# Kernel tuning notes

Hardware: AMD Instinct MI355X
Metric: run time of the kernel (lower is better)

## Reference

```python
import jax, jax.numpy as jnp
import numpy as np

B, N, D, OUT, ED = 8, 256, 128, 128, 1

def setup_inputs() -> dict:
    key = jax.random.key(0)
    ks = jax.random.split(key, 10)
    in2 = 2 * D + ED  # 257
    s = lambda f: 1.0 / np.sqrt(f)
    return {
        "h": jax.random.normal(ks[0], (B, N, D), dtype=jnp.float32),
        "adj": jax.random.randint(ks[1], (B, N, N), 0, 2, dtype=jnp.int32),
        "dist_matrix": jax.random.uniform(ks[2], (B, N, N), dtype=jnp.float32),
        "Wm1": jax.random.uniform(ks[3], (in2, OUT), minval=-s(in2), maxval=s(in2)),
        "bm1": jnp.zeros((OUT,), jnp.float32),
        "Wm2": jax.random.uniform(ks[4], (OUT, OUT), minval=-s(OUT), maxval=s(OUT)),
        "bm2": jnp.zeros((OUT,), jnp.float32),
        "Wa": jax.random.uniform(ks[5], (in2, 1), minval=-s(in2), maxval=s(in2)),
        "ba": jnp.zeros((1,), jnp.float32),
        "Wu": jax.random.uniform(ks[6], (D + OUT, OUT), minval=-s(D + OUT), maxval=s(D + OUT)),
        "bu": jnp.zeros((OUT,), jnp.float32),
    }

def reference(h, adj, dist_matrix, Wm1, bm1, Wm2, bm2, Wa, ba, Wu, bu):
    # h: (B,N,D); adj,dist: (B,N,N)
    Bb, Nn, Dd = h.shape
    h_i = jnp.broadcast_to(h[:, :, None, :], (Bb, Nn, Nn, Dd))
    h_j = jnp.broadcast_to(h[:, None, :, :], (Bb, Nn, Nn, Dd))
    d_ij = dist_matrix[..., None]
    msg_input = jnp.concatenate([h_i, h_j, d_ij], axis=-1)  # (B,N,N,2D+1)
    # message MLP: Linear -> ReLU -> Linear
    msg = jax.nn.relu(msg_input @ Wm1 + bm1) @ Wm2 + bm2    # (B,N,N,OUT)
    # attention MLP: Linear -> LeakyReLU(0.2)
    attn = jax.nn.leaky_relu(msg_input @ Wa + ba, 0.2)      # (B,N,N,1)
    mask = adj[..., None].astype(msg.dtype)                  # (B,N,N,1)
    attn = jnp.where(mask == 0, jnp.asarray(-1e9, attn.dtype), attn)
    attn = jax.nn.softmax(attn, axis=2)                      # softmax over j
    agg = jnp.sum(attn * msg * mask, axis=2)                 # (B,N,OUT)
    h_new = jax.nn.relu(jnp.concatenate([h, agg], axis=-1) @ Wu + bu)
    return h_new
```

## Files before the change

### kernel.cpp

```cpp
#include <hip/hip_runtime.h>

#define NN 256
#define DD 128
#define OC 128

__device__ __forceinline__ float bcastf(float x, int lane) {
    return __int_as_float(__builtin_amdgcn_readlane(__float_as_int(x), lane));
}

__global__ __launch_bounds__(256) void k1_pre(
    const float* __restrict__ h, const float* __restrict__ Wm1,
    const float* __restrict__ Wa, const float* __restrict__ bm1,
    const float* __restrict__ Wu, const float* __restrict__ ba,
    float* __restrict__ pre, float* __restrict__ aiv, float* __restrict__ ajv)
{
    const int tid  = threadIdx.x;
    const int l    = tid & 63;
    const int w    = tid >> 6;
    const int row0 = blockIdx.x * 2;

    const float2* h2 = (const float2*)h;
    float2 hr[2];
    hr[0] = h2[row0 * 64 + l];
    hr[1] = h2[(row0 + 1) * 64 + l];

    if (w == 3) {
        const float2* Wa2 = (const float2*)Wa;
        const float2 wt = Wa2[l], wb = Wa2[64 + l];
        float vi[2], vj[2];
        #pragma unroll
        for (int r = 0; r < 2; ++r) {
            vi[r] = hr[r].x * wt.x + hr[r].y * wt.y;
            vj[r] = hr[r].x * wb.x + hr[r].y * wb.y;
        }
        #pragma unroll
        for (int o = 1; o < 64; o <<= 1) {
            #pragma unroll
            for (int r = 0; r < 2; ++r) {
                vi[r] += __shfl_xor(vi[r], o, 64);
                vj[r] += __shfl_xor(vj[r], o, 64);
            }
        }
        if (l == 0) {
            const float b0 = ba[0];
            #pragma unroll
            for (int r = 0; r < 2; ++r) {
                aiv[row0 + r] = vi[r] + b0;
                ajv[row0 + r] = vj[r];
            }
        }
        return;
    }

    const float2* W2 = (w == 0) ? (const float2*)Wm1
                     : (w == 1) ? (const float2*)Wm1 + DD * 64
                                : (const float2*)Wu;

    float2 acc[2] = {{0.f, 0.f}, {0.f, 0.f}};
    #pragma unroll 8
    for (int m = 0; m < 64; ++m) {
        const float2 w0 = W2[(2 * m) * 64 + l];
        const float2 w1 = W2[(2 * m + 1) * 64 + l];
        #pragma unroll
        for (int r = 0; r < 2; ++r) {
            const float hx = bcastf(hr[r].x, m);
            const float hy = bcastf(hr[r].y, m);
            acc[r].x = fmaf(hx, w0.x, fmaf(hy, w1.x, acc[r].x));
            acc[r].y = fmaf(hx, w0.y, fmaf(hy, w1.y, acc[r].y));
        }
    }
    if (w == 0) {
        const float2 bb = ((const float2*)bm1)[l];
        #pragma unroll
        for (int r = 0; r < 2; ++r) { acc[r].x += bb.x; acc[r].y += bb.y; }
    }
    float2* pre2 = (float2*)pre;
    #pragma unroll
    for (int r = 0; r < 2; ++r)
        pre2[(row0 + r) * 192 + w * 64 + l] = acc[r];
}

__global__ __launch_bounds__(256) void k2_main(
    const int* __restrict__ adj, const float* __restrict__ dist,
    const float* __restrict__ Wm1, const float* __restrict__ Wa,
    const float* __restrict__ pre,
    const float* __restrict__ aiv, const float* __restrict__ ajv,
    const float* __restrict__ Wm2, const float* __restrict__ bm2,
    const float* __restrict__ Wu,  const float* __restrict__ bu,
    float* __restrict__ out)
{
    const int tid  = threadIdx.x;
    const int l    = tid & 63;
    const int wid  = tid >> 6;
    const int r    = wid >> 1;
    const int hf   = wid & 1;
    const int row0 = blockIdx.x * 2;
    const int row  = row0 + r;
    const int b    = row >> 8;

    __shared__ float mx_sh[4], sm_sh[4], sf_sh[2];
    __shared__ float tp_sh[4][128];
    __shared__ float t_sh[2][128];
    __shared__ float agg_sh[2][128];

    const float2 dv2 = ((const float2*)(dist + row * NN))[hf * 64 + l];
    const int2   mk2 = ((const int2*)  (adj  + row * NN))[hf * 64 + l];
    const float2 aj2 = ((const float2*)(ajv  + b   * NN))[hf * 64 + l];
    const float  ai  = aiv[row];
    const float  dc  = Wa[2 * DD];

    float l0 = ai + aj2.x + dv2.x * dc;
    float l1 = ai + aj2.y + dv2.y * dc;
    l0 = (l0 >= 0.f) ? l0 : 0.2f * l0;
    l1 = (l1 >= 0.f) ? l1 : 0.2f * l1;

    float m = fmaxf(mk2.x ? l0 : -1e9f, mk2.y ? l1 : -1e9f);
    #pragma unroll
    for (int o = 1; o < 64; o <<= 1) m = fmaxf(m, __shfl_xor(m, o, 64));
    if (l == 0) mx_sh[wid] = m;
    __syncthreads();
    const float mx = fmaxf(mx_sh[r * 2], mx_sh[r * 2 + 1]);

    const float e0 = mk2.x ? __expf(l0 - mx) : 0.f;
    const float e1 = mk2.y ? __expf(l1 - mx) : 0.f;
    float s = e0 + e1;
    #pragma unroll
    for (int o = 1; o < 64; o <<= 1) s += __shfl_xor(s, o, 64);
    if (l == 0) sm_sh[wid] = s;
    __syncthreads();
    const float esum = sm_sh[r * 2] + sm_sh[r * 2 + 1];
    const float inv  = (esum > 0.f) ? (1.0f / esum) : 0.f;
    const float w0 = e0 * inv, w1 = e1 * inv;

    const float2* pre2 = (const float2*)pre;
    const float2  pa   = pre2[row * 192 + l];
    const float2  wd1  = ((const float2*)Wm1)[2 * DD * 64 + l];
    const float2* pBb  = pre2 + (size_t)b * NN * 192 + 64 + (size_t)hf * 128 * 192;

    float2 acc = make_float2(0.f, 0.f);
    #pragma unroll 8
    for (int p = 0; p < 64; ++p) {
        const float w0p = bcastf(w0, p);
        const float w1p = bcastf(w1, p);
        const float d0p = bcastf(dv2.x, p);
        const float d1p = bcastf(dv2.y, p);
        const float2 pb0 = pBb[(2 * p) * 192 + l];
        const float2 pb1 = pBb[(2 * p + 1) * 192 + l];
        float vx = fmaf(d0p, wd1.x, pa.x + pb0.x);
        float vy = fmaf(d0p, wd1.y, pa.y + pb0.y);
        acc.x = fmaf(w0p, fmaxf(vx, 0.f), acc.x);
        acc.y = fmaf(w0p, fmaxf(vy, 0.f), acc.y);
        vx = fmaf(d1p, wd1.x, pa.x + pb1.x);
        vy = fmaf(d1p, wd1.y, pa.y + pb1.y);
        acc.x = fmaf(w1p, fmaxf(vx, 0.f), acc.x);
        acc.y = fmaf(w1p, fmaxf(vy, 0.f), acc.y);
    }
    tp_sh[wid][2 * l]     = acc.x;
    tp_sh[wid][2 * l + 1] = acc.y;
    if (l == 0 && hf == 0) sf_sh[r] = (esum > 0.f) ? 1.f : 0.f;
    __syncthreads();

    {
        const int rr = tid >> 7, cc = tid & 127;
        t_sh[rr][cc] = tp_sh[rr * 2][cc] + tp_sh[rr * 2 + 1][cc];
    }
    __syncthreads();

    const int r2 = tid >> 7, c = tid & 127;
    float av = 0.f;
    #pragma unroll 8
    for (int k = 0; k < 128; ++k)
        av = fmaf(t_sh[r2][k], Wm2[k * OC + c], av);
    agg_sh[r2][c] = fmaf(bm2[c], sf_sh[r2], av);
    __syncthreads();

    float ov = 0.f;
    #pragma unroll 8
    for (int k = 0; k < 128; ++k)
        ov = fmaf(agg_sh[r2][k], Wu[(DD + k) * OC + c], ov);
    const float hu = pre[(row0 + r2) * 384 + 256 + c];
    out[(row0 + r2) * OC + c] = fmaxf(ov + hu + bu[c], 0.f);
}

extern "C" void kernel_launch(void* const* d_in, const int* in_sizes, int n_in,
                              void* d_out, int out_size, void* d_ws, size_t ws_size,
                              hipStream_t stream) {
    const float* h    = (const float*)d_in[0];
    const int*   adj  = (const int*)  d_in[1];
    const float* dist = (const float*)d_in[2];
    const float* Wm1  = (const float*)d_in[3];
    const float* bm1  = (const float*)d_in[4];
    const float* Wm2  = (const float*)d_in[5];
    const float* bm2  = (const float*)d_in[6];
    const float* Wa   = (const float*)d_in[7];
    const float* ba   = (const float*)d_in[8];
    const float* Wu   = (const float*)d_in[9];
    const float* bu   = (const float*)d_in[10];
    float* out = (float*)d_out;

    float* pre = (float*)d_ws;
    float* aiv = pre + 2048 * 384;
    float* ajv = aiv + 2048;

    k1_pre <<<1024, 256, 0, stream>>>(h, Wm1, Wa, bm1, Wu, ba, pre, aiv, ajv);
    k2_main<<<1024, 256, 0, stream>>>(adj, dist, Wm1, Wa, pre, aiv, ajv,
                                      Wm2, bm2, Wu, bu, out);
}
```

Before: 116.4 us.

## Remap k2 to one row per block and vectorize k1 weight loads

k2_main now processes one output row per block, with each of its four waves covering 64 neighbor columns, and launches 2048 blocks instead of 1024. The two small 128x128 matvecs are split along k across the two half-blocks and reduced through shared memory. k1_pre switches to float4 weight loads, splitting the input dimension across half-waves and combining them with a cross-half shuffle. Launch-bounds occupancy hints are added. This buys more parallelism and wider loads at the cost of extra syncs and some repeated per-block work.

After: 112.1 us. 3.7% less time.

```diff
diff --git a/kernel.cpp b/kernel.cpp
--- a/kernel.cpp
+++ b/kernel.cpp
@@ -8,7 +8,7 @@
     return __int_as_float(__builtin_amdgcn_readlane(__float_as_int(x), lane));
 }
 
-__global__ __launch_bounds__(256) void k1_pre(
+__global__ __launch_bounds__(256, 4) void k1_pre(
     const float* __restrict__ h, const float* __restrict__ Wm1,
     const float* __restrict__ Wa, const float* __restrict__ bm1,
     const float* __restrict__ Wu, const float* __restrict__ ba,
@@ -20,67 +20,68 @@
     const int row0 = blockIdx.x * 2;
 
     const float2* h2 = (const float2*)h;
-    float2 hr[2];
-    hr[0] = h2[row0 * 64 + l];
-    hr[1] = h2[(row0 + 1) * 64 + l];
+    const float2 hr0 = h2[row0 * 64 + l];
+    const float2 hr1 = h2[(row0 + 1) * 64 + l];
 
     if (w == 3) {
         const float2* Wa2 = (const float2*)Wa;
         const float2 wt = Wa2[l], wb = Wa2[64 + l];
-        float vi[2], vj[2];
-        #pragma unroll
-        for (int r = 0; r < 2; ++r) {
-            vi[r] = hr[r].x * wt.x + hr[r].y * wt.y;
-            vj[r] = hr[r].x * wb.x + hr[r].y * wb.y;
-        }
+        float vi0 = hr0.x * wt.x + hr0.y * wt.y;
+        float vj0 = hr0.x * wb.x + hr0.y * wb.y;
+        float vi1 = hr1.x * wt.x + hr1.y * wt.y;
+        float vj1 = hr1.x * wb.x + hr1.y * wb.y;
         #pragma unroll
         for (int o = 1; o < 64; o <<= 1) {
-            #pragma unroll
-            for (int r = 0; r < 2; ++r) {
-                vi[r] += __shfl_xor(vi[r], o, 64);
-                vj[r] += __shfl_xor(vj[r], o, 64);
-            }
+            vi0 += __shfl_xor(vi0, o, 64);
+            vj0 += __shfl_xor(vj0, o, 64);
+            vi1 += __shfl_xor(vi1, o, 64);
+            vj1 += __shfl_xor(vj1, o, 64);
         }
         if (l == 0) {
             const float b0 = ba[0];
-            #pragma unroll
-            for (int r = 0; r < 2; ++r) {
-                aiv[row0 + r] = vi[r] + b0;
-                ajv[row0 + r] = vj[r];
-            }
+            aiv[row0]     = vi0 + b0;  ajv[row0]     = vj0;
+            aiv[row0 + 1] = vi1 + b0;  ajv[row0 + 1] = vj1;
         }
         return;
     }
 
-    const float2* W2 = (w == 0) ? (const float2*)Wm1
-                     : (w == 1) ? (const float2*)Wm1 + DD * 64
-                                : (const float2*)Wu;
-
-    float2 acc[2] = {{0.f, 0.f}, {0.f, 0.f}};
-    #pragma unroll 8
-    for (int m = 0; m < 64; ++m) {
-        const float2 w0 = W2[(2 * m) * 64 + l];
-        const float2 w1 = W2[(2 * m + 1) * 64 + l];
-        #pragma unroll
-        for (int r = 0; r < 2; ++r) {
-            const float hx = bcastf(hr[r].x, m);
-            const float hy = bcastf(hr[r].y, m);
-            acc[r].x = fmaf(hx, w0.x, fmaf(hy, w1.x, acc[r].x));
-            acc[r].y = fmaf(hx, w0.y, fmaf(hy, w1.y, acc[r].y));
+    const float* Wbase = (w == 0) ? Wm1 : (w == 1) ? (Wm1 + DD * OC) : Wu;
+    const float4* W4 = (const float4*)Wbase;
+    const int dsel = l >> 5;
+    const int q    = l & 31;
+
+    float4 a0 = {0.f, 0.f, 0.f, 0.f};
+    float4 a1 = {0.f, 0.f, 0.f, 0.f};
+    #pragma unroll 8
+    for (int i = 0; i < 64; ++i) {
+        const float4 wv = W4[(2 * i + dsel) * 32 + q];
+        const float h0e = bcastf(hr0.x, i), h0o = bcastf(hr0.y, i);
+        const float h1e = bcastf(hr1.x, i), h1o = bcastf(hr1.y, i);
+        const float hx0 = dsel ? h0o : h0e;
+        const float hx1 = dsel ? h1o : h1e;
+        a0.x = fmaf(hx0, wv.x, a0.x); a0.y = fmaf(hx0, wv.y, a0.y);
+        a0.z = fmaf(hx0, wv.z, a0.z); a0.w = fmaf(hx0, wv.w, a0.w);
+        a1.x = fmaf(hx1, wv.x, a1.x); a1.y = fmaf(hx1, wv.y, a1.y);
+        a1.z = fmaf(hx1, wv.z, a1.z); a1.w = fmaf(hx1, wv.w, a1.w);
+    }
+    a0.x += __shfl_xor(a0.x, 32, 64); a0.y += __shfl_xor(a0.y, 32, 64);
+    a0.z += __shfl_xor(a0.z, 32, 64); a0.w += __shfl_xor(a0.w, 32, 64);
+    a1.x += __shfl_xor(a1.x, 32, 64); a1.y += __shfl_xor(a1.y, 32, 64);
+    a1.z += __shfl_xor(a1.z, 32, 64); a1.w += __shfl_xor(a1.w, 32, 64);
+
+    if (l < 32) {
+        if (w == 0) {
+            const float4 bb = ((const float4*)bm1)[q];
+            a0.x += bb.x; a0.y += bb.y; a0.z += bb.z; a0.w += bb.w;
+            a1.x += bb.x; a1.y += bb.y; a1.z += bb.z; a1.w += bb.w;
         }
-    }
-    if (w == 0) {
-        const float2 bb = ((const float2*)bm1)[l];
-        #pragma unroll
-        for (int r = 0; r < 2; ++r) { acc[r].x += bb.x; acc[r].y += bb.y; }
-    }
-    float2* pre2 = (float2*)pre;
-    #pragma unroll
-    for (int r = 0; r < 2; ++r)
-        pre2[(row0 + r) * 192 + w * 64 + l] = acc[r];
-}
-
-__global__ __launch_bounds__(256) void k2_main(
+        float4* pre4 = (float4*)pre;
+        pre4[row0 * 96 + w * 32 + q]       = a0;
+        pre4[(row0 + 1) * 96 + w * 32 + q] = a1;
+    }
+}
+
+__global__ __launch_bounds__(256, 8) void k2_main(
     const int* __restrict__ adj, const float* __restrict__ dist,
     const float* __restrict__ Wm1, const float* __restrict__ Wa,
     const float* __restrict__ pre,
@@ -89,97 +90,93 @@
     const float* __restrict__ Wu,  const float* __restrict__ bu,
     float* __restrict__ out)
 {
-    const int tid  = threadIdx.x;
-    const int l    = tid & 63;
-    const int wid  = tid >> 6;
-    const int r    = wid >> 1;
-    const int hf   = wid & 1;
-    const int row0 = blockIdx.x * 2;
-    const int row  = row0 + r;
-    const int b    = row >> 8;
-
-    __shared__ float mx_sh[4], sm_sh[4], sf_sh[2];
+    const int tid = threadIdx.x;
+    const int l   = tid & 63;
+    const int wid = tid >> 6;
+    const int row = blockIdx.x;
+    const int b   = row >> 8;
+
+    __shared__ float mx_sh[4], sm_sh[4];
     __shared__ float tp_sh[4][128];
-    __shared__ float t_sh[2][128];
-    __shared__ float agg_sh[2][128];
-
-    const float2 dv2 = ((const float2*)(dist + row * NN))[hf * 64 + l];
-    const int2   mk2 = ((const int2*)  (adj  + row * NN))[hf * 64 + l];
-    const float2 aj2 = ((const float2*)(ajv  + b   * NN))[hf * 64 + l];
-    const float  ai  = aiv[row];
-    const float  dc  = Wa[2 * DD];
-
-    float l0 = ai + aj2.x + dv2.x * dc;
-    float l1 = ai + aj2.y + dv2.y * dc;
-    l0 = (l0 >= 0.f) ? l0 : 0.2f * l0;
-    l1 = (l1 >= 0.f) ? l1 : 0.2f * l1;
-
-    float m = fmaxf(mk2.x ? l0 : -1e9f, mk2.y ? l1 : -1e9f);
+    __shared__ float t_sh[128];
+    __shared__ float agg_sh[128];
+
+    const int   j  = 64 * wid + l;
+    const float dv = dist[row * NN + j];
+    const int   mk = adj[row * NN + j];
+    const float ajl = ajv[b * NN + j];
+    const float ai  = aiv[row];
+    const float dc  = Wa[2 * DD];
+
+    float lg = ai + ajl + dv * dc;
+    lg = (lg >= 0.f) ? lg : 0.2f * lg;
+
+    float m = mk ? lg : -1e9f;
     #pragma unroll
     for (int o = 1; o < 64; o <<= 1) m = fmaxf(m, __shfl_xor(m, o, 64));
     if (l == 0) mx_sh[wid] = m;
     __syncthreads();
-    const float mx = fmaxf(mx_sh[r * 2], mx_sh[r * 2 + 1]);
-
-    const float e0 = mk2.x ? __expf(l0 - mx) : 0.f;
-    const float e1 = mk2.y ? __expf(l1 - mx) : 0.f;
-    float s = e0 + e1;
+    const float mx = fmaxf(fmaxf(mx_sh[0], mx_sh[1]), fmaxf(mx_sh[2], mx_sh[3]));
+
+    const float e = mk ? __expf(lg - mx) : 0.f;
+    float s = e;
     #pragma unroll
     for (int o = 1; o < 64; o <<= 1) s += __shfl_xor(s, o, 64);
     if (l == 0) sm_sh[wid] = s;
     __syncthreads();
-    const float esum = sm_sh[r * 2] + sm_sh[r * 2 + 1];
+    const float esum = sm_sh[0] + sm_sh[1] + sm_sh[2] + sm_sh[3];
     const float inv  = (esum > 0.f) ? (1.0f / esum) : 0.f;
-    const float w0 = e0 * inv, w1 = e1 * inv;
+    const float wj   = e * inv;
+    const float sf   = (esum > 0.f) ? 1.f : 0.f;
 
     const float2* pre2 = (const float2*)pre;
     const float2  pa   = pre2[row * 192 + l];
     const float2  wd1  = ((const float2*)Wm1)[2 * DD * 64 + l];
-    const float2* pBb  = pre2 + (size_t)b * NN * 192 + 64 + (size_t)hf * 128 * 192;
-
-    float2 acc = make_float2(0.f, 0.f);
+    const float2* pBb  = pre2 + (size_t)b * NN * 192 + 64;
+    const int     jb   = 64 * wid;
+
+    float2 acc = {0.f, 0.f};
     #pragma unroll 8
     for (int p = 0; p < 64; ++p) {
-        const float w0p = bcastf(w0, p);
-        const float w1p = bcastf(w1, p);
-        const float d0p = bcastf(dv2.x, p);
-        const float d1p = bcastf(dv2.y, p);
-        const float2 pb0 = pBb[(2 * p) * 192 + l];
-        const float2 pb1 = pBb[(2 * p + 1) * 192 + l];
-        float vx = fmaf(d0p, wd1.x, pa.x + pb0.x);
-        float vy = fmaf(d0p, wd1.y, pa.y + pb0.y);
-        acc.x = fmaf(w0p, fmaxf(vx, 0.f), acc.x);
-        acc.y = fmaf(w0p, fmaxf(vy, 0.f), acc.y);
-        vx = fmaf(d1p, wd1.x, pa.x + pb1.x);
-        vy = fmaf(d1p, wd1.y, pa.y + pb1.y);
-        acc.x = fmaf(w1p, fmaxf(vx, 0.f), acc.x);
-        acc.y = fmaf(w1p, fmaxf(vy, 0.f), acc.y);
+        const float wp = bcastf(wj, p);
+        const float dp = bcastf(dv, p);
+        const float2 pb = pBb[(jb + p) * 192 + l];
+        const float vx = fmaf(dp, wd1.x, pa.x + pb.x);
+        const float vy = fmaf(dp, wd1.y, pa.y + pb.y);
+        acc.x = fmaf(wp, fmaxf(vx, 0.f), acc.x);
+        acc.y = fmaf(wp, fmaxf(vy, 0.f), acc.y);
     }
     tp_sh[wid][2 * l]     = acc.x;
     tp_sh[wid][2 * l + 1] = acc.y;
-    if (l == 0 && hf == 0) sf_sh[r] = (esum > 0.f) ? 1.f : 0.f;
-    __syncthreads();
-
-    {
-        const int rr = tid >> 7, cc = tid & 127;
-        t_sh[rr][cc] = tp_sh[rr * 2][cc] + tp_sh[rr * 2 + 1][cc];
-    }
-    __syncthreads();
-
-    const int r2 = tid >> 7, c = tid & 127;
-    float av = 0.f;
-    #pragma unroll 8
-    for (int k = 0; k < 128; ++k)
-        av = fmaf(t_sh[r2][k], Wm2[k * OC + c], av);
-    agg_sh[r2][c] = fmaf(bm2[c], sf_sh[r2], av);
-    __syncthreads();
-
-    float ov = 0.f;
-    #pragma unroll 8
-    for (int k = 0; k < 128; ++k)
-        ov = fmaf(agg_sh[r2][k], Wu[(DD + k) * OC + c], ov);
-    const float hu = pre[(row0 + r2) * 384 + 256 + c];
-    out[(row0 + r2) * OC + c] = fmaxf(ov + hu + bu[c], 0.f);
+    __syncthreads();
+    if (tid < 128)
+        t_sh[tid] = tp_sh[0][tid] + tp_sh[1][tid] + tp_sh[2][tid] + tp_sh[3][tid];
+    __syncthreads();
+
+    const int kh = tid >> 7, c = tid & 127;
+    float pc = 0.f;
+    #pragma unroll 8
+    for (int k = 0; k < 64; ++k) {
+        const int kk = 64 * kh + k;
+        pc = fmaf(t_sh[kk], Wm2[kk * OC + c], pc);
+    }
+    tp_sh[kh][c] = pc;
+    __syncthreads();
+    if (tid < 128) agg_sh[tid] = tp_sh[0][tid] + tp_sh[1][tid] + bm2[tid] * sf;
+    __syncthreads();
+
+    float pd = 0.f;
+    #pragma unroll 8
+    for (int k = 0; k < 64; ++k) {
+        const int kk = 64 * kh + k;
+        pd = fmaf(agg_sh[kk], Wu[(DD + kk) * OC + c], pd);
+    }
+    tp_sh[kh][c] = pd;
+    __syncthreads();
+    if (tid < 128) {
+        const float hu = pre[row * 384 + 256 + tid];
+        out[row * OC + tid] = fmaxf(tp_sh[0][tid] + tp_sh[1][tid] + hu + bu[tid], 0.f);
+    }
 }
 
 extern "C" void kernel_launch(void* const* d_in, const int* in_sizes, int n_in,
@@ -203,6 +200,6 @@
     float* ajv = aiv + 2048;
 
     k1_pre <<<1024, 256, 0, stream>>>(h, Wm1, Wa, bm1, Wu, ba, pre, aiv, ajv);
-    k2_main<<<1024, 256, 0, stream>>>(adj, dist, Wm1, Wa, pre, aiv, ajv,
+    k2_main<<<2048, 256, 0, stream>>>(adj, dist, Wm1, Wa, pre, aiv, ajv,
                                       Wm2, bm2, Wu, bu, out);
 }
```

## Stage per-batch j-projection in LDS and process eight rows per block

Applied to the files above, without the earlier changes.

k2 now loads the whole 256x128 h_j projection for a batch into shared memory once per block and handles 8 rows per block (one wave per row), removing repeated global/L2 reads of that tile and the cross-wave softmax reductions. k1 processes 8 rows per block with float4 weight loads split across half-waves to raise weight reuse. Grids shrink to 256 blocks; the large LDS footprint limits occupancy to one block per CU and the staging load is not overlapped with compute.

Result: faster. 109.9 us (-5.6%).

```diff
diff --git a/kernel.cpp b/kernel.cpp
--- a/kernel.cpp
+++ b/kernel.cpp
@@ -8,7 +8,7 @@
     return __int_as_float(__builtin_amdgcn_readlane(__float_as_int(x), lane));
 }
 
-__global__ __launch_bounds__(256) void k1_pre(
+__global__ __launch_bounds__(256, 2) void k1_pre(
     const float* __restrict__ h, const float* __restrict__ Wm1,
     const float* __restrict__ Wa, const float* __restrict__ bm1,
     const float* __restrict__ Wu, const float* __restrict__ ba,
@@ -17,26 +17,26 @@
     const int tid  = threadIdx.x;
     const int l    = tid & 63;
     const int w    = tid >> 6;
-    const int row0 = blockIdx.x * 2;
+    const int row0 = blockIdx.x * 8;
 
     const float2* h2 = (const float2*)h;
-    float2 hr[2];
-    hr[0] = h2[row0 * 64 + l];
-    hr[1] = h2[(row0 + 1) * 64 + l];
+    float2 hr[8];
+    #pragma unroll
+    for (int r = 0; r < 8; ++r) hr[r] = h2[(row0 + r) * 64 + l];
 
     if (w == 3) {
         const float2* Wa2 = (const float2*)Wa;
         const float2 wt = Wa2[l], wb = Wa2[64 + l];
-        float vi[2], vj[2];
-        #pragma unroll
-        for (int r = 0; r < 2; ++r) {
+        float vi[8], vj[8];
+        #pragma unroll
+        for (int r = 0; r < 8; ++r) {
             vi[r] = hr[r].x * wt.x + hr[r].y * wt.y;
             vj[r] = hr[r].x * wb.x + hr[r].y * wb.y;
         }
         #pragma unroll
         for (int o = 1; o < 64; o <<= 1) {
             #pragma unroll
-            for (int r = 0; r < 2; ++r) {
+            for (int r = 0; r < 8; ++r) {
                 vi[r] += __shfl_xor(vi[r], o, 64);
                 vj[r] += __shfl_xor(vj[r], o, 64);
             }
@@ -44,7 +44,7 @@
         if (l == 0) {
             const float b0 = ba[0];
             #pragma unroll
-            for (int r = 0; r < 2; ++r) {
+            for (int r = 0; r < 8; ++r) {
                 aiv[row0 + r] = vi[r] + b0;
                 ajv[row0 + r] = vj[r];
             }
@@ -52,35 +52,53 @@
         return;
     }
 
-    const float2* W2 = (w == 0) ? (const float2*)Wm1
-                     : (w == 1) ? (const float2*)Wm1 + DD * 64
-                                : (const float2*)Wu;
-
-    float2 acc[2] = {{0.f, 0.f}, {0.f, 0.f}};
-    #pragma unroll 8
-    for (int m = 0; m < 64; ++m) {
-        const float2 w0 = W2[(2 * m) * 64 + l];
-        const float2 w1 = W2[(2 * m + 1) * 64 + l];
-        #pragma unroll
-        for (int r = 0; r < 2; ++r) {
-            const float hx = bcastf(hr[r].x, m);
-            const float hy = bcastf(hr[r].y, m);
-            acc[r].x = fmaf(hx, w0.x, fmaf(hy, w1.x, acc[r].x));
-            acc[r].y = fmaf(hx, w0.y, fmaf(hy, w1.y, acc[r].y));
-        }
-    }
-    if (w == 0) {
-        const float2 bb = ((const float2*)bm1)[l];
-        #pragma unroll
-        for (int r = 0; r < 2; ++r) { acc[r].x += bb.x; acc[r].y += bb.y; }
-    }
-    float2* pre2 = (float2*)pre;
-    #pragma unroll
-    for (int r = 0; r < 2; ++r)
-        pre2[(row0 + r) * 192 + w * 64 + l] = acc[r];
-}
-
-__global__ __launch_bounds__(256) void k2_main(
+    const float* Wbase = (w == 0) ? Wm1 : (w == 1) ? (Wm1 + DD * OC) : Wu;
+    const float4* W4 = (const float4*)Wbase;
+    const int dsel = l >> 5;
+    const int q    = l & 31;
+
+    float4 a[8];
+    #pragma unroll
+    for (int r = 0; r < 8; ++r) a[r] = make_float4(0.f, 0.f, 0.f, 0.f);
+
+    #pragma unroll 4
+    for (int i = 0; i < 64; ++i) {
+        const float4 wv = W4[(2 * i + dsel) * 32 + q];
+        #pragma unroll
+        for (int r = 0; r < 8; ++r) {
+            const float he = bcastf(hr[r].x, i);
+            const float ho = bcastf(hr[r].y, i);
+            const float hx = dsel ? ho : he;
+            a[r].x = fmaf(hx, wv.x, a[r].x);
+            a[r].y = fmaf(hx, wv.y, a[r].y);
+            a[r].z = fmaf(hx, wv.z, a[r].z);
+            a[r].w = fmaf(hx, wv.w, a[r].w);
+        }
+    }
+    #pragma unroll
+    for (int r = 0; r < 8; ++r) {
+        a[r].x += __shfl_xor(a[r].x, 32, 64);
+        a[r].y += __shfl_xor(a[r].y, 32, 64);
+        a[r].z += __shfl_xor(a[r].z, 32, 64);
+        a[r].w += __shfl_xor(a[r].w, 32, 64);
+    }
+
+    if (l < 32) {
+        if (w == 0) {
+            const float4 bb = ((const float4*)bm1)[q];
+            #pragma unroll
+            for (int r = 0; r < 8; ++r) {
+                a[r].x += bb.x; a[r].y += bb.y; a[r].z += bb.z; a[r].w += bb.w;
+            }
+        }
+        float4* pre4 = (float4*)pre;
+        #pragma unroll
+        for (int r = 0; r < 8; ++r)
+            pre4[(row0 + r) * 96 + w * 32 + q] = a[r];
+    }
+}
+
+__global__ __launch_bounds__(512, 2) void k2_main(
     const int* __restrict__ adj, const float* __restrict__ dist,
     const float* __restrict__ Wm1, const float* __restrict__ Wa,
     const float* __restrict__ pre,
@@ -92,94 +110,112 @@
     const int tid  = threadIdx.x;
     const int l    = tid & 63;
     const int wid  = tid >> 6;
-    const int r    = wid >> 1;
-    const int hf   = wid & 1;
-    const int row0 = blockIdx.x * 2;
-    const int row  = row0 + r;
-    const int b    = row >> 8;
-
-    __shared__ float mx_sh[4], sm_sh[4], sf_sh[2];
-    __shared__ float tp_sh[4][128];
-    __shared__ float t_sh[2][128];
-    __shared__ float agg_sh[2][128];
-
-    const float2 dv2 = ((const float2*)(dist + row * NN))[hf * 64 + l];
-    const int2   mk2 = ((const int2*)  (adj  + row * NN))[hf * 64 + l];
-    const float2 aj2 = ((const float2*)(ajv  + b   * NN))[hf * 64 + l];
+    const int row0 = blockIdx.x * 8;
+    const int row  = row0 + wid;
+    const int b    = row0 >> 8;
+
+    __shared__ float pB[NN][128];
+    __shared__ float t_sh[8][128];
+    __shared__ float agg_sh[8][128];
+    __shared__ float sf_sh[8];
+
+    {
+        const float4* pre4 = (const float4*)pre;
+        const int q  = tid & 31;
+        const int jr = tid >> 5;
+        #pragma unroll
+        for (int it = 0; it < 16; ++it) {
+            const int j = jr * 16 + it;
+            ((float4*)pB[j])[q] = pre4[(b * NN + j) * 96 + 32 + q];
+        }
+    }
+
+    const int4   mk4 = ((const int4*)  (adj  + row * NN))[l];
+    const float4 dv4 = ((const float4*)(dist + row * NN))[l];
+    const float4 aj4 = ((const float4*)(ajv  + b   * NN))[l];
     const float  ai  = aiv[row];
     const float  dc  = Wa[2 * DD];
 
-    float l0 = ai + aj2.x + dv2.x * dc;
-    float l1 = ai + aj2.y + dv2.y * dc;
-    l0 = (l0 >= 0.f) ? l0 : 0.2f * l0;
-    l1 = (l1 >= 0.f) ? l1 : 0.2f * l1;
-
-    float m = fmaxf(mk2.x ? l0 : -1e9f, mk2.y ? l1 : -1e9f);
+    float lg0 = ai + aj4.x + dv4.x * dc;
+    float lg1 = ai + aj4.y + dv4.y * dc;
+    float lg2 = ai + aj4.z + dv4.z * dc;
+    float lg3 = ai + aj4.w + dv4.w * dc;
+    lg0 = (lg0 >= 0.f) ? lg0 : 0.2f * lg0;
+    lg1 = (lg1 >= 0.f) ? lg1 : 0.2f * lg1;
+    lg2 = (lg2 >= 0.f) ? lg2 : 0.2f * lg2;
+    lg3 = (lg3 >= 0.f) ? lg3 : 0.2f * lg3;
+
+    float m = fmaxf(fmaxf(mk4.x ? lg0 : -1e9f, mk4.y ? lg1 : -1e9f),
+                    fmaxf(mk4.z ? lg2 : -1e9f, mk4.w ? lg3 : -1e9f));
     #pragma unroll
     for (int o = 1; o < 64; o <<= 1) m = fmaxf(m, __shfl_xor(m, o, 64));
-    if (l == 0) mx_sh[wid] = m;
-    __syncthreads();
-    const float mx = fmaxf(mx_sh[r * 2], mx_sh[r * 2 + 1]);
-
-    const float e0 = mk2.x ? __expf(l0 - mx) : 0.f;
-    const float e1 = mk2.y ? __expf(l1 - mx) : 0.f;
-    float s = e0 + e1;
+
+    const float e0 = mk4.x ? __expf(lg0 - m) : 0.f;
+    const float e1 = mk4.y ? __expf(lg1 - m) : 0.f;
+    const float e2 = mk4.z ? __expf(lg2 - m) : 0.f;
+    const float e3 = mk4.w ? __expf(lg3 - m) : 0.f;
+    float s = e0 + e1 + e2 + e3;
     #pragma unroll
     for (int o = 1; o < 64; o <<= 1) s += __shfl_xor(s, o, 64);
-    if (l == 0) sm_sh[wid] = s;
-    __syncthreads();
-    const float esum = sm_sh[r * 2] + sm_sh[r * 2 + 1];
-    const float inv  = (esum > 0.f) ? (1.0f / esum) : 0.f;
-    const float w0 = e0 * inv, w1 = e1 * inv;
+    const float inv = (s > 0.f) ? (1.0f / s) : 0.f;
+    const float w0 = e0 * inv, w1 = e1 * inv, w2 = e2 * inv, w3 = e3 * inv;
+    if (l == 0) sf_sh[wid] = (s > 0.f) ? 1.f : 0.f;
 
     const float2* pre2 = (const float2*)pre;
     const float2  pa   = pre2[row * 192 + l];
     const float2  wd1  = ((const float2*)Wm1)[2 * DD * 64 + l];
-    const float2* pBb  = pre2 + (size_t)b * NN * 192 + 64 + (size_t)hf * 128 * 192;
-
-    float2 acc = make_float2(0.f, 0.f);
+    __syncthreads();
+
+    float2 acc = {0.f, 0.f};
+    #define PHB(WW, DV, CC)                                          \
+    {                                                                \
+        _Pragma("unroll 8")                                          \
+        for (int p = 0; p < 64; ++p) {                               \
+            const float wp = bcastf(WW, p);                          \
+            const float dp = bcastf(DV, p);                          \
+            const float2 pb = ((const float2*)pB[4 * p + CC])[l];    \
+            const float vx = fmaf(dp, wd1.x, pa.x + pb.x);           \
+            const float vy = fmaf(dp, wd1.y, pa.y + pb.y);           \
+            acc.x = fmaf(wp, fmaxf(vx, 0.f), acc.x);                 \
+            acc.y = fmaf(wp, fmaxf(vy, 0.f), acc.y);                 \
+        }                                                            \
+    }
+    PHB(w0, dv4.x, 0)
+    PHB(w1, dv4.y, 1)
+    PHB(w2, dv4.z, 2)
+    PHB(w3, dv4.w, 3)
+    #undef PHB
+
+    t_sh[wid][2 * l]     = acc.x;
+    t_sh[wid][2 * l + 1] = acc.y;
+    __syncthreads();
+
+    const int c  = tid & 127;
+    const int rh = tid >> 7;
+    float c0 = 0.f, c1 = 0.f;
     #pragma unroll 8
-    for (int p = 0; p < 64; ++p) {
-        const float w0p = bcastf(w0, p);
-        const float w1p = bcastf(w1, p);
-        const float d0p = bcastf(dv2.x, p);
-        const float d1p = bcastf(dv2.y, p);
-        const float2 pb0 = pBb[(2 * p) * 192 + l];
-        const float2 pb1 = pBb[(2 * p + 1) * 192 + l];
-        float vx = fmaf(d0p, wd1.x, pa.x + pb0.x);
-        float vy = fmaf(d0p, wd1.y, pa.y + pb0.y);
-        acc.x = fmaf(w0p, fmaxf(vx, 0.f), acc.x);
-        acc.y = fmaf(w0p, fmaxf(vy, 0.f), acc.y);
-        vx = fmaf(d1p, wd1.x, pa.x + pb1.x);
-        vy = fmaf(d1p, wd1.y, pa.y + pb1.y);
-        acc.x = fmaf(w1p, fmaxf(vx, 0.f), acc.x);
-        acc.y = fmaf(w1p, fmaxf(vy, 0.f), acc.y);
-    }
-    tp_sh[wid][2 * l]     = acc.x;
-    tp_sh[wid][2 * l + 1] = acc.y;
-    if (l == 0 && hf == 0) sf_sh[r] = (esum > 0.f) ? 1.f : 0.f;
+    for (int k = 0; k < 128; ++k) {
+        const float wv = Wm2[k * OC + c];
+        c0 = fmaf(t_sh[rh][k],     wv, c0);
+        c1 = fmaf(t_sh[rh + 4][k], wv, c1);
+    }
+    const float bmc = bm2[c];
+    agg_sh[rh][c]     = fmaf(bmc, sf_sh[rh],     c0);
+    agg_sh[rh + 4][c] = fmaf(bmc, sf_sh[rh + 4], c1);
     __syncthreads();
 
-    {
-        const int rr = tid >> 7, cc = tid & 127;
-        t_sh[rr][cc] = tp_sh[rr * 2][cc] + tp_sh[rr * 2 + 1][cc];
-    }
-    __syncthreads();
-
-    const int r2 = tid >> 7, c = tid & 127;
-    float av = 0.f;
+    float d0 = 0.f, d1 = 0.f;
     #pragma unroll 8
-    for (int k = 0; k < 128; ++k)
-        av = fmaf(t_sh[r2][k], Wm2[k * OC + c], av);
-    agg_sh[r2][c] = fmaf(bm2[c], sf_sh[r2], av);
-    __syncthreads();
-
-    float ov = 0.f;
-    #pragma unroll 8
-    for (int k = 0; k < 128; ++k)
-        ov = fmaf(agg_sh[r2][k], Wu[(DD + k) * OC + c], ov);
-    const float hu = pre[(row0 + r2) * 384 + 256 + c];
-    out[(row0 + r2) * OC + c] = fmaxf(ov + hu + bu[c], 0.f);
+    for (int k = 0; k < 128; ++k) {
+        const float wv = Wu[(DD + k) * OC + c];
+        d0 = fmaf(agg_sh[rh][k],     wv, d0);
+        d1 = fmaf(agg_sh[rh + 4][k], wv, d1);
+    }
+    const float buc = bu[c];
+    const float hu0 = pre[(row0 + rh) * 384 + 256 + c];
+    const float hu1 = pre[(row0 + rh + 4) * 384 + 256 + c];
+    out[(row0 + rh) * OC + c]     = fmaxf(d0 + hu0 + buc, 0.f);
+    out[(row0 + rh + 4) * OC + c] = fmaxf(d1 + hu1 + buc, 0.f);
 }
 
 extern "C" void kernel_launch(void* const* d_in, const int* in_sizes, int n_in,
@@ -202,7 +238,7 @@
     float* aiv = pre + 2048 * 384;
     float* ajv = aiv + 2048;
 
-    k1_pre <<<1024, 256, 0, stream>>>(h, Wm1, Wa, bm1, Wu, ba, pre, aiv, ajv);
-    k2_main<<<1024, 256, 0, stream>>>(adj, dist, Wm1, Wa, pre, aiv, ajv,
-                                      Wm2, bm2, Wu, bu, out);
-}
+    k1_pre <<<256, 256, 0, stream>>>(h, Wm1, Wa, bm1, Wu, ba, pre, aiv, ajv);
+    k2_main<<<256, 512, 0, stream>>>(adj, dist, Wm1, Wa, pre, aiv, ajv,
+                                     Wm2, bm2, Wu, bu, out);
+}
```

## Store per-node hj projection as bf16 and stage it in LDS per block

Applied to the files above, without the earlier changes.

The first kernel now processes four rows per block with float4 weight loads. It writes the h_j projection of Wm1 as bf16 into a separate buffer. The main kernel uses 512-thread blocks covering four rows and copies the batch's entire bf16 projection table (64 KB) into shared memory. The pair loop then reads from LDS instead of re-reading fp32 rows from global memory. This halves the gather traffic and adds reuse across rows, at the cost of bf16 rounding, a large LDS footprint that limits occupancy, and a per-block staging copy.

Result: faster. 108.5 us, median of 2 (-6.8%).

```diff
diff --git a/kernel.cpp b/kernel.cpp
--- a/kernel.cpp
+++ b/kernel.cpp
@@ -7,36 +7,42 @@
 __device__ __forceinline__ float bcastf(float x, int lane) {
     return __int_as_float(__builtin_amdgcn_readlane(__float_as_int(x), lane));
 }
-
-__global__ __launch_bounds__(256) void k1_pre(
+__device__ __forceinline__ unsigned short f2bf(float x) {
+    unsigned int u = __float_as_uint(x);
+    u = (u + 0x7fffu + ((u >> 16) & 1u)) >> 16;
+    return (unsigned short)u;
+}
+
+__global__ __launch_bounds__(256, 4) void k1_pre(
     const float* __restrict__ h, const float* __restrict__ Wm1,
     const float* __restrict__ Wa, const float* __restrict__ bm1,
     const float* __restrict__ Wu, const float* __restrict__ ba,
-    float* __restrict__ pre, float* __restrict__ aiv, float* __restrict__ ajv)
+    float* __restrict__ pre, unsigned short* __restrict__ pbB,
+    float* __restrict__ aiv, float* __restrict__ ajv)
 {
     const int tid  = threadIdx.x;
     const int l    = tid & 63;
     const int w    = tid >> 6;
-    const int row0 = blockIdx.x * 2;
+    const int row0 = blockIdx.x * 4;
 
     const float2* h2 = (const float2*)h;
-    float2 hr[2];
-    hr[0] = h2[row0 * 64 + l];
-    hr[1] = h2[(row0 + 1) * 64 + l];
+    float2 hr[4];
+    #pragma unroll
+    for (int r = 0; r < 4; ++r) hr[r] = h2[(row0 + r) * 64 + l];
 
     if (w == 3) {
         const float2* Wa2 = (const float2*)Wa;
         const float2 wt = Wa2[l], wb = Wa2[64 + l];
-        float vi[2], vj[2];
-        #pragma unroll
-        for (int r = 0; r < 2; ++r) {
+        float vi[4], vj[4];
+        #pragma unroll
+        for (int r = 0; r < 4; ++r) {
             vi[r] = hr[r].x * wt.x + hr[r].y * wt.y;
             vj[r] = hr[r].x * wb.x + hr[r].y * wb.y;
         }
         #pragma unroll
         for (int o = 1; o < 64; o <<= 1) {
             #pragma unroll
-            for (int r = 0; r < 2; ++r) {
+            for (int r = 0; r < 4; ++r) {
                 vi[r] += __shfl_xor(vi[r], o, 64);
                 vj[r] += __shfl_xor(vj[r], o, 64);
             }
@@ -44,7 +50,7 @@
         if (l == 0) {
             const float b0 = ba[0];
             #pragma unroll
-            for (int r = 0; r < 2; ++r) {
+            for (int r = 0; r < 4; ++r) {
                 aiv[row0 + r] = vi[r] + b0;
                 ajv[row0 + r] = vj[r];
             }
@@ -52,38 +58,68 @@
         return;
     }
 
-    const float2* W2 = (w == 0) ? (const float2*)Wm1
-                     : (w == 1) ? (const float2*)Wm1 + DD * 64
-                                : (const float2*)Wu;
-
-    float2 acc[2] = {{0.f, 0.f}, {0.f, 0.f}};
-    #pragma unroll 8
-    for (int m = 0; m < 64; ++m) {
-        const float2 w0 = W2[(2 * m) * 64 + l];
-        const float2 w1 = W2[(2 * m + 1) * 64 + l];
-        #pragma unroll
-        for (int r = 0; r < 2; ++r) {
-            const float hx = bcastf(hr[r].x, m);
-            const float hy = bcastf(hr[r].y, m);
-            acc[r].x = fmaf(hx, w0.x, fmaf(hy, w1.x, acc[r].x));
-            acc[r].y = fmaf(hx, w0.y, fmaf(hy, w1.y, acc[r].y));
-        }
-    }
-    if (w == 0) {
-        const float2 bb = ((const float2*)bm1)[l];
-        #pragma unroll
-        for (int r = 0; r < 2; ++r) { acc[r].x += bb.x; acc[r].y += bb.y; }
-    }
-    float2* pre2 = (float2*)pre;
-    #pragma unroll
-    for (int r = 0; r < 2; ++r)
-        pre2[(row0 + r) * 192 + w * 64 + l] = acc[r];
-}
-
-__global__ __launch_bounds__(256) void k2_main(
+    const float* Wbase = (w == 0) ? Wm1 : (w == 1) ? (Wm1 + DD * OC) : Wu;
+    const float4* W4 = (const float4*)Wbase;
+    const int dsel = l >> 5;
+    const int q    = l & 31;
+
+    float4 a[4];
+    #pragma unroll
+    for (int r = 0; r < 4; ++r) a[r] = make_float4(0.f, 0.f, 0.f, 0.f);
+
+    #pragma unroll 8
+    for (int i = 0; i < 64; ++i) {
+        const float4 wv = W4[(2 * i + dsel) * 32 + q];
+        #pragma unroll
+        for (int r = 0; r < 4; ++r) {
+            const float he = bcastf(hr[r].x, i);
+            const float ho = bcastf(hr[r].y, i);
+            const float hx = dsel ? ho : he;
+            a[r].x = fmaf(hx, wv.x, a[r].x);
+            a[r].y = fmaf(hx, wv.y, a[r].y);
+            a[r].z = fmaf(hx, wv.z, a[r].z);
+            a[r].w = fmaf(hx, wv.w, a[r].w);
+        }
+    }
+    #pragma unroll
+    for (int r = 0; r < 4; ++r) {
+        a[r].x += __shfl_xor(a[r].x, 32, 64);
+        a[r].y += __shfl_xor(a[r].y, 32, 64);
+        a[r].z += __shfl_xor(a[r].z, 32, 64);
+        a[r].w += __shfl_xor(a[r].w, 32, 64);
+    }
+
+    if (l < 32) {
+        if (w == 1) {
+            #pragma unroll
+            for (int r = 0; r < 4; ++r) {
+                ushort4 p;
+                p.x = f2bf(a[r].x); p.y = f2bf(a[r].y);
+                p.z = f2bf(a[r].z); p.w = f2bf(a[r].w);
+                ((ushort4*)pbB)[(row0 + r) * 32 + q] = p;
+            }
+        } else {
+            float4* pre4 = (float4*)pre;
+            const int roff = (w == 0) ? 0 : 32;
+            if (w == 0) {
+                const float4 bb = ((const float4*)bm1)[q];
+                #pragma unroll
+                for (int r = 0; r < 4; ++r) {
+                    a[r].x += bb.x; a[r].y += bb.y;
+                    a[r].z += bb.z; a[r].w += bb.w;
+                }
+            }
+            #pragma unroll
+            for (int r = 0; r < 4; ++r)
+                pre4[(row0 + r) * 64 + roff + q] = a[r];
+        }
+    }
+}
+
+__global__ __launch_bounds__(512, 4) void k2_main(
     const int* __restrict__ adj, const float* __restrict__ dist,
     const float* __restrict__ Wm1, const float* __restrict__ Wa,
-    const float* __restrict__ pre,
+    const float* __restrict__ pre, const unsigned short* __restrict__ pbB,
     const float* __restrict__ aiv, const float* __restrict__ ajv,
     const float* __restrict__ Wm2, const float* __restrict__ bm2,
     const float* __restrict__ Wu,  const float* __restrict__ bu,
@@ -94,17 +130,26 @@
     const int wid  = tid >> 6;
     const int r    = wid >> 1;
     const int hf   = wid & 1;
-    const int row0 = blockIdx.x * 2;
+    const int row0 = blockIdx.x * 4;
     const int row  = row0 + r;
-    const int b    = row >> 8;
-
-    __shared__ float mx_sh[4], sm_sh[4], sf_sh[2];
-    __shared__ float tp_sh[4][128];
-    __shared__ float t_sh[2][128];
-    __shared__ float agg_sh[2][128];
-
+    const int b    = row0 >> 8;
+
+    __shared__ unsigned int pB[NN * 64];
+    __shared__ float mx_sh[8], sm_sh[8], sf_sh[4];
+    __shared__ float tp_sh[8][128];
+    __shared__ float t_sh[4][128];
+    __shared__ float agg_sh[4][128];
+
+    {
+        const uint4* src = (const uint4*)(pbB + (size_t)b * NN * 128);
+        uint4* dst = (uint4*)pB;
+        #pragma unroll
+        for (int it = 0; it < 8; ++it)
+            dst[tid + 512 * it] = src[tid + 512 * it];
+    }
+
+    const int2   mk2 = ((const int2*)  (adj  + row * NN))[hf * 64 + l];
     const float2 dv2 = ((const float2*)(dist + row * NN))[hf * 64 + l];
-    const int2   mk2 = ((const int2*)  (adj  + row * NN))[hf * 64 + l];
     const float2 aj2 = ((const float2*)(ajv  + b   * NN))[hf * 64 + l];
     const float  ai  = aiv[row];
     const float  dc  = Wa[2 * DD];
@@ -119,7 +164,7 @@
     for (int o = 1; o < 64; o <<= 1) m = fmaxf(m, __shfl_xor(m, o, 64));
     if (l == 0) mx_sh[wid] = m;
     __syncthreads();
-    const float mx = fmaxf(mx_sh[r * 2], mx_sh[r * 2 + 1]);
+    const float mx = fmaxf(mx_sh[2 * r], mx_sh[2 * r + 1]);
 
     const float e0 = mk2.x ? __expf(l0 - mx) : 0.f;
     const float e1 = mk2.y ? __expf(l1 - mx) : 0.f;
@@ -128,58 +173,62 @@
     for (int o = 1; o < 64; o <<= 1) s += __shfl_xor(s, o, 64);
     if (l == 0) sm_sh[wid] = s;
     __syncthreads();
-    const float esum = sm_sh[r * 2] + sm_sh[r * 2 + 1];
+    const float esum = sm_sh[2 * r] + sm_sh[2 * r + 1];
     const float inv  = (esum > 0.f) ? (1.0f / esum) : 0.f;
     const float w0 = e0 * inv, w1 = e1 * inv;
-
-    const float2* pre2 = (const float2*)pre;
-    const float2  pa   = pre2[row * 192 + l];
-    const float2  wd1  = ((const float2*)Wm1)[2 * DD * 64 + l];
-    const float2* pBb  = pre2 + (size_t)b * NN * 192 + 64 + (size_t)hf * 128 * 192;
-
-    float2 acc = make_float2(0.f, 0.f);
+    if (l == 0 && hf == 0) sf_sh[r] = (esum > 0.f) ? 1.f : 0.f;
+
+    const float2 pa  = ((const float2*)(pre + row * 256))[l];
+    const float2 wd1 = ((const float2*)Wm1)[2 * DD * 64 + l];
+    const unsigned int* pBh = pB + (hf * 128) * 64;
+
+    float2 acc = {0.f, 0.f};
     #pragma unroll 8
     for (int p = 0; p < 64; ++p) {
         const float w0p = bcastf(w0, p);
+        const float d0p = bcastf(dv2.x, p);
         const float w1p = bcastf(w1, p);
-        const float d0p = bcastf(dv2.x, p);
         const float d1p = bcastf(dv2.y, p);
-        const float2 pb0 = pBb[(2 * p) * 192 + l];
-        const float2 pb1 = pBb[(2 * p + 1) * 192 + l];
-        float vx = fmaf(d0p, wd1.x, pa.x + pb0.x);
-        float vy = fmaf(d0p, wd1.y, pa.y + pb0.y);
-        acc.x = fmaf(w0p, fmaxf(vx, 0.f), acc.x);
-        acc.y = fmaf(w0p, fmaxf(vy, 0.f), acc.y);
-        vx = fmaf(d1p, wd1.x, pa.x + pb1.x);
-        vy = fmaf(d1p, wd1.y, pa.y + pb1.y);
-        acc.x = fmaf(w1p, fmaxf(vx, 0.f), acc.x);
-        acc.y = fmaf(w1p, fmaxf(vy, 0.f), acc.y);
+        const unsigned int u0 = pBh[(2 * p) * 64 + l];
+        const unsigned int u1 = pBh[(2 * p + 1) * 64 + l];
+        {
+            const float pbx = __uint_as_float(u0 << 16);
+            const float pby = __uint_as_float(u0 & 0xffff0000u);
+            const float vx = fmaf(d0p, wd1.x, pa.x + pbx);
+            const float vy = fmaf(d0p, wd1.y, pa.y + pby);
+            acc.x = fmaf(w0p, fmaxf(vx, 0.f), acc.x);
+            acc.y = fmaf(w0p, fmaxf(vy, 0.f), acc.y);
+        }
+        {
+            const float pbx = __uint_as_float(u1 << 16);
+            const float pby = __uint_as_float(u1 & 0xffff0000u);
+            const float vx = fmaf(d1p, wd1.x, pa.x + pbx);
+            const float vy = fmaf(d1p, wd1.y, pa.y + pby);
+            acc.x = fmaf(w1p, fmaxf(vx, 0.f), acc.x);
+            acc.y = fmaf(w1p, fmaxf(vy, 0.f), acc.y);
+        }
     }
     tp_sh[wid][2 * l]     = acc.x;
     tp_sh[wid][2 * l + 1] = acc.y;
-    if (l == 0 && hf == 0) sf_sh[r] = (esum > 0.f) ? 1.f : 0.f;
-    __syncthreads();
-
-    {
-        const int rr = tid >> 7, cc = tid & 127;
-        t_sh[rr][cc] = tp_sh[rr * 2][cc] + tp_sh[rr * 2 + 1][cc];
-    }
-    __syncthreads();
-
-    const int r2 = tid >> 7, c = tid & 127;
+    __syncthreads();
+
+    const int rr = tid >> 7, cc = tid & 127;
+    t_sh[rr][cc] = tp_sh[2 * rr][cc] + tp_sh[2 * rr + 1][cc];
+    __syncthreads();
+
     float av = 0.f;
     #pragma unroll 8
     for (int k = 0; k < 128; ++k)
-        av = fmaf(t_sh[r2][k], Wm2[k * OC + c], av);
-    agg_sh[r2][c] = fmaf(bm2[c], sf_sh[r2], av);
+        av = fmaf(t_sh[rr][k], Wm2[k * OC + cc], av);
+    agg_sh[rr][cc] = fmaf(bm2[cc], sf_sh[rr], av);
     __syncthreads();
 
     float ov = 0.f;
     #pragma unroll 8
     for (int k = 0; k < 128; ++k)
-        ov = fmaf(agg_sh[r2][k], Wu[(DD + k) * OC + c], ov);
-    const float hu = pre[(row0 + r2) * 384 + 256 + c];
-    out[(row0 + r2) * OC + c] = fmaxf(ov + hu + bu[c], 0.f);
+        ov = fmaf(agg_sh[rr][k], Wu[(DD + k) * OC + cc], ov);
+    const float hu = pre[(row0 + rr) * 256 + 128 + cc];
+    out[(row0 + rr) * OC + cc] = fmaxf(ov + hu + bu[cc], 0.f);
 }
 
 extern "C" void kernel_launch(void* const* d_in, const int* in_sizes, int n_in,
@@ -198,11 +247,12 @@
     const float* bu   = (const float*)d_in[10];
     float* out = (float*)d_out;
 
-    float* pre = (float*)d_ws;
-    float* aiv = pre + 2048 * 384;
-    float* ajv = aiv + 2048;
-
-    k1_pre <<<1024, 256, 0, stream>>>(h, Wm1, Wa, bm1, Wu, ba, pre, aiv, ajv);
-    k2_main<<<1024, 256, 0, stream>>>(adj, dist, Wm1, Wa, pre, aiv, ajv,
-                                      Wm2, bm2, Wu, bu, out);
-}
+    float*          pre = (float*)d_ws;
+    unsigned short* pbB = (unsigned short*)(pre + 2048 * 256);
+    float*          aiv = (float*)(pbB + 2048 * 128);
+    float*          ajv = aiv + 2048;
+
+    k1_pre <<<512, 256, 0, stream>>>(h, Wm1, Wa, bm1, Wu, ba, pre, pbB, aiv, ajv);
+    k2_main<<<512, 512, 0, stream>>>(adj, dist, Wm1, Wa, pre, pbB, aiv, ajv,
+                                     Wm2, bm2, Wu, bu, out);
+}
```
